# Optimization experiments

Hardware: AMD Instinct MI355X
Metric: run time of the kernel (lower is better)

## Reference

```python
import jax, jax.numpy as jnp
import numpy as np

B, DIM, H, W = 2, 192, 64, 64
HEADS = 4
EPS = 1e-12  # torch F.normalize eps


def conv2d(x, w, groups=1):
    # x: NCHW, w: OIHW, stride 1, SAME padding
    return jax.lax.conv_general_dilated(
        x, w, window_strides=(1, 1), padding='SAME',
        feature_group_count=groups,
        dimension_numbers=('NCHW', 'OIHW', 'NCHW'))


def setup_inputs() -> dict:
    key = jax.random.key(0)
    k1, k2, k3, k4 = jax.random.split(key, 4)
    x = jax.random.normal(k1, (B, DIM, H, W), dtype=jnp.float32)
    qkv_w = jax.random.normal(k2, (3 * DIM, DIM, 1, 1), dtype=jnp.float32) * 0.05
    dw_w = jax.random.normal(k3, (3 * DIM, 1, 3, 3), dtype=jnp.float32) * 0.05
    proj_w = jax.random.normal(k4, (DIM, DIM, 1, 1), dtype=jnp.float32) * 0.05
    temperature = jnp.ones((HEADS, 1, 1), dtype=jnp.float32)
    return {'x': x, 'qkv_w': qkv_w, 'dw_w': dw_w, 'proj_w': proj_w,
            'temperature': temperature}


def reference(x, qkv_w, dw_w, proj_w, temperature):
    b, dim, h, w = x.shape
    heads = temperature.shape[0]
    c = dim // heads  # per-head channels

    qkv = conv2d(conv2d(x, qkv_w), dw_w, groups=3 * dim)  # [b, 3*dim, h, w]
    q, k, v = jnp.split(qkv, 3, axis=1)

    def to_heads(t):
        # b (head c) h w -> b head (h w) c
        return t.reshape(b, heads, c, h * w).transpose(0, 1, 3, 2)

    q, k, v = to_heads(q), to_heads(k), to_heads(v)

    def l2norm(t):
        n = jnp.linalg.norm(t, axis=-1, keepdims=True)
        return t / jnp.maximum(n, EPS)

    q = l2norm(q)
    k = l2norm(k)

    # cosine attention with per-head learnable temperature
    attn = jnp.einsum('bnqc,bnkc->bnqk', q, k) * temperature[None]
    attn = jax.nn.softmax(attn, axis=-1)
    out = jnp.einsum('bnqk,bnkc->bnqc', attn, v)  # [b, head, hw, c]

    # b head (h w) c -> b (head c) h w
    out = out.transpose(0, 1, 3, 2).reshape(b, dim, h, w)
    return conv2d(out, proj_w)
```

## Files before the change

### kernel.cpp

```cpp
#include <hip/hip_runtime.h>
#include <cstdint>
#include <cstddef>

#define HW    4096
#define IMG   64
#define DIMC  192
#define NH    4
#define CH    48
#define CPAD  64
#define KVSPLIT 4
#define NTILE (HW / 64 / KVSPLIT)
#define LOG2E 1.4426950408889634f

typedef __bf16 bf16x8 __attribute__((ext_vector_type(8)));
typedef float  f32x4  __attribute__((ext_vector_type(4)));
typedef float  f32x16 __attribute__((ext_vector_type(16)));
typedef unsigned short u16x8 __attribute__((ext_vector_type(8)));
typedef unsigned int   u32x4 __attribute__((ext_vector_type(4)));

#if __has_builtin(__builtin_amdgcn_exp2f)
#define EXP2(x) __builtin_amdgcn_exp2f(x)
#else
#define EXP2(x) exp2f(x)
#endif

__device__ __forceinline__ unsigned short f2bf(float f) {
  unsigned int u = __builtin_bit_cast(unsigned int, f);
  u = (u + 0x7FFFu + ((u >> 16) & 1u)) >> 16;
  return (unsigned short)u;
}
__device__ __forceinline__ float bf2f(unsigned short u) {
  return __builtin_bit_cast(float, (unsigned int)u << 16);
}
__device__ __forceinline__ f32x4 mfma16(bf16x8 a, bf16x8 b, f32x4 c) {
  return __builtin_amdgcn_mfma_f32_16x16x32_bf16(a, b, c, 0, 0, 0);
}
__device__ __forceinline__ f32x16 mfma32(bf16x8 a, bf16x8 b, f32x16 c) {
  return __builtin_amdgcn_mfma_f32_32x32x16_bf16(a, b, c, 0, 0, 0);
}
__device__ __forceinline__ void gl16(const void* g, void* l) {
  __builtin_amdgcn_global_load_lds(
      (const __attribute__((address_space(1))) unsigned int*)g,
      (__attribute__((address_space(3))) unsigned int*)l, 16, 0, 0);
}
__device__ __forceinline__ unsigned int cvtpk(float lo, float hi) {
  unsigned int d;
  asm("v_cvt_pk_bf16_f32 %0, %1, %2" : "=v"(d) : "v"(lo), "v"(hi));
  return d;
}
__device__ __forceinline__ void swap32(unsigned int& a, unsigned int& b) {
  asm("v_permlane32_swap_b32 %0, %1" : "+v"(a), "+v"(b));
}

__global__ __launch_bounds__(256) void pack2_kernel(
    const float* __restrict__ x, const float* __restrict__ qkv_w,
    const float* __restrict__ proj_w, unsigned short* __restrict__ xb,
    unsigned short* __restrict__ wqkv, unsigned short* __restrict__ wproj) {
  const int bx = blockIdx.x, tid = threadIdx.x;
  if (bx < 64) {
    const int half = bx & 1;
    const int gpx = (bx >> 1) * 256 + tid;
    const int b = gpx >> 12, p = gpx & 4095;
    const int ch0 = half * 96;
    const float* src = x + ((size_t)b * DIMC + ch0) * HW + p;
    #pragma unroll
    for (int kc2 = 0; kc2 < 3; ++kc2) {
      const int kc = half * 3 + kc2;
      u16x8 g[4];
      #pragma unroll
      for (int v = 0; v < 4; ++v)
        #pragma unroll
        for (int j = 0; j < 8; ++j)
          g[v][j] = f2bf(src[(size_t)(kc2 * 32 + v * 8 + j) * HW]);
      unsigned short* dst = xb + (((size_t)b * 6 + kc) * HW + p) * 32;
      #pragma unroll
      for (int v = 0; v < 4; ++v) *(u16x8*)(dst + v * 8) = g[v];
    }
  } else {
    const int row = (bx - 64) * 256 + tid;
    if (row < 576) {
      const float* src = qkv_w + (size_t)row * DIMC;
      #pragma unroll
      for (int kc = 0; kc < 6; ++kc) {
        u16x8 g0, g1, g2, g3;
        #pragma unroll
        for (int j = 0; j < 8; ++j) {
          g0[j] = f2bf(src[kc * 32 + j]);      g1[j] = f2bf(src[kc * 32 + 8 + j]);
          g2[j] = f2bf(src[kc * 32 + 16 + j]); g3[j] = f2bf(src[kc * 32 + 24 + j]);
        }
        unsigned short* dst = wqkv + ((size_t)kc * 576 + row) * 32;
        *(u16x8*)dst = g0; *(u16x8*)(dst + 8) = g1;
        *(u16x8*)(dst + 16) = g2; *(u16x8*)(dst + 24) = g3;
      }
    } else {
      const int oc = row - 576;
      const float* src = proj_w + (size_t)oc * DIMC;
      #pragma unroll
      for (int kc = 0; kc < 6; ++kc) {
        u16x8 g0, g1, g2, g3;
        #pragma unroll
        for (int j = 0; j < 8; ++j) {
          g0[j] = f2bf(src[kc * 32 + j]);      g1[j] = f2bf(src[kc * 32 + 8 + j]);
          g2[j] = f2bf(src[kc * 32 + 16 + j]); g3[j] = f2bf(src[kc * 32 + 24 + j]);
        }
        unsigned short* dst = wproj + ((size_t)kc * DIMC + oc) * 32;
        *(u16x8*)dst = g0; *(u16x8*)(dst + 8) = g1;
        *(u16x8*)(dst + 16) = g2; *(u16x8*)(dst + 24) = g3;
      }
    }
  }
}

__global__ __launch_bounds__(256) void qkv_gemm_kernel(
    const unsigned short* __restrict__ xb, const unsigned short* __restrict__ wb,
    unsigned short* __restrict__ Cout) {
  const int tid = threadIdx.x;
  const int lane = tid & 63, wv = tid >> 6;
  const int l15 = lane & 15, l4 = lane >> 4;
  const int ocbase = blockIdx.x * 192;
  const int px0 = blockIdx.y * 64;
  const int b   = blockIdx.z;

  f32x4 acc[3][4];
  #pragma unroll
  for (int s = 0; s < 3; ++s)
    #pragma unroll
    for (int p = 0; p < 4; ++p) acc[s][p] = f32x4{0.f, 0.f, 0.f, 0.f};

  #pragma unroll
  for (int kc = 0; kc < 6; ++kc) {
    const unsigned short* xrow = xb + (((size_t)b * 6 + kc) * HW + px0 + l15) * 32 + l4 * 8;
    bf16x8 Bf[4];
    #pragma unroll
    for (int p = 0; p < 4; ++p) Bf[p] = *(const bf16x8*)(xrow + p * 512);
    #pragma unroll
    for (int s = 0; s < 3; ++s) {
      const int oc = ocbase + s * 64 + wv * 16 + l15;
      const bf16x8 af = *(const bf16x8*)(wb + ((size_t)kc * 576 + oc) * 32 + l4 * 8);
      #pragma unroll
      for (int p = 0; p < 4; ++p) acc[s][p] = mfma16(af, Bf[p], acc[s][p]);
    }
  }
  #pragma unroll
  for (int s = 0; s < 3; ++s) {
    unsigned short* Cb = Cout + ((size_t)b * 576 + ocbase + s * 64 + wv * 16) * HW + px0;
    #pragma unroll
    for (int p = 0; p < 4; ++p)
      #pragma unroll
      for (int r = 0; r < 4; ++r)
        Cb[(size_t)(l4 * 4 + r) * HW + p * 16 + l15] = f2bf(acc[s][p][r]);
  }
}

__global__ __launch_bounds__(256) void dw_conv3_kernel(
    const unsigned short* __restrict__ X, const float* __restrict__ W,
    unsigned short* __restrict__ Y) {
  __shared__ float T[66][72];
  const int bc = blockIdx.x;
  const int ch = bc % 576;
  const int tid = threadIdx.x;
  const unsigned short* Xb = X + (size_t)bc * HW;
  #pragma unroll
  for (int i = 0; i < 4; ++i) {
    const int idx = i * 256 + tid;
    const int row = idx >> 4, c4 = (idx & 15) << 2;
    const ushort4 u = *(const ushort4*)(Xb + row * 64 + c4);
    float4 f; f.x = bf2f(u.x); f.y = bf2f(u.y); f.z = bf2f(u.z); f.w = bf2f(u.w);
    *(float4*)&T[row + 1][c4 + 4] = f;
  }
  if (tid < 72) { T[0][tid] = 0.f; T[65][tid] = 0.f; }
  if (tid >= 128 && tid < 194) { const int r = tid - 128; T[r][3] = 0.f; T[r][68] = 0.f; }
  float w[9];
  #pragma unroll
  for (int i = 0; i < 9; ++i) w[i] = W[ch * 9 + i];
  __syncthreads();

  const int xx = tid & 63, ys = (tid >> 6) << 4;
  const int c = xx + 4;
  float a0 = T[ys][c - 1],     a1 = T[ys][c],     a2 = T[ys][c + 1];
  float b0 = T[ys + 1][c - 1], b1 = T[ys + 1][c], b2 = T[ys + 1][c + 1];
  unsigned short* Yb = Y + (size_t)bc * HW;
  #pragma unroll
  for (int k = 0; k < 16; ++k) {
    const float c0 = T[ys + k + 2][c - 1], c1 = T[ys + k + 2][c], c2 = T[ys + k + 2][c + 1];
    const float s = w[0] * a0 + w[1] * a1 + w[2] * a2
                  + w[3] * b0 + w[4] * b1 + w[5] * b2
                  + w[6] * c0 + w[7] * c1 + w[8] * c2;
    Yb[(ys + k) * 64 + xx] = f2bf(s);
    a0 = b0; a1 = b1; a2 = b2; b0 = c0; b1 = c1; b2 = c2;
  }
}

__global__ __launch_bounds__(256) void norm_pack3_kernel(
    const unsigned short* __restrict__ Dw, const float* __restrict__ temp,
    unsigned short* __restrict__ Qr, unsigned short* __restrict__ Kr,
    unsigned short* __restrict__ Vs) {
  const int px = blockIdx.x * 256 + threadIdx.x;
  const int sel = blockIdx.y >> 2, h = blockIdx.y & 3;
  const int b = blockIdx.z;
  const int bh = b * NH + h;
  const unsigned short* base = Dw + ((size_t)b * 576 + sel * DIMC + h * CH) * HW + px;

  float v[CH];
  if (sel == 2) {
    const int kt = px & ~63, kl = px & 63;
    #pragma unroll
    for (int c = 0; c < CH; ++c)
      Vs[((size_t)bh * CH + c) * HW + kt + (kl ^ ((c & 7) << 3))] = base[(size_t)c * HW];
    return;
  }
  float ss = 0.f;
  #pragma unroll
  for (int j = 0; j < CH; ++j) { v[j] = bf2f(base[(size_t)j * HW]); ss += v[j] * v[j]; }
  const u16x8 zz = {0, 0, 0, 0, 0, 0, 0, 0};
  if (sel == 0) {
    const float sc = temp[h] * LOG2E / fmaxf(sqrtf(ss), 1e-12f);
    u16x8 gr[8];
    #pragma unroll
    for (int g = 0; g < 6; ++g)
      #pragma unroll
      for (int j = 0; j < 8; ++j) gr[g][j] = f2bf(v[g * 8 + j] * sc);
    gr[6] = zz; gr[7] = zz;
    unsigned short* qrow = Qr + ((size_t)bh * HW + px) * CPAD;
    #pragma unroll
    for (int g = 0; g < 8; ++g) *(u16x8*)(qrow + g * 8) = gr[g];
  } else {
    const int ksw = (px & 3) | (((px >> 3) & 1) << 2);
    const float sc = 1.0f / fmaxf(sqrtf(ss), 1e-12f);
    u16x8 gr[8];
    #pragma unroll
    for (int g = 0; g < 6; ++g)
      #pragma unroll
      for (int j = 0; j < 8; ++j) gr[g][j] = f2bf(v[g * 8 + j] * sc);
    gr[6] = zz; gr[7] = zz;
    unsigned short* krow = Kr + ((size_t)bh * HW + px) * CPAD;
    #pragma unroll
    for (int g = 0; g < 8; ++g) *(u16x8*)(krow + (g ^ ksw) * 8) = gr[g];
  }
}

__global__ __launch_bounds__(256, 2) void flash7_kernel(
    const unsigned short* __restrict__ Qr,
    const unsigned short* __restrict__ Kr,
    const unsigned short* __restrict__ Vs,
    const float* __restrict__ temp,
    unsigned short* __restrict__ Opart, float* __restrict__ Lpart) {
  __shared__ __align__(16) union {
    struct { unsigned short Kl[2][4096]; unsigned short Vl[2][4096]; } s;
    float T[256][53];
  } lds;
  const int tid = threadIdx.x;
  const int lane = tid & 63, wv = tid >> 6;
  const int l31 = lane & 31, lhi = lane >> 5;
  const int bh = blockIdx.x, qt = blockIdx.y, sp = blockIdx.z;
  const int qb = qt * 256 + wv * 64;
  const float m = fabsf(temp[bh & 3]) * LOG2E * 1.05f + 0.1f;

  for (int i = tid; i < 1024; i += 256) {
    const unsigned short vv = (i < 64) ? (unsigned short)0x3F80 : (unsigned short)0;
    lds.s.Vl[0][3072 + i] = vv;
    lds.s.Vl[1][3072 + i] = vv;
  }

  const unsigned short* Qb = Qr + ((size_t)bh * HW + qb) * CPAD;
  bf16x8 qf[2][3];
  #pragma unroll
  for (int qb2 = 0; qb2 < 2; ++qb2)
    #pragma unroll
    for (int ci = 0; ci < 3; ++ci)
      qf[qb2][ci] = *(const bf16x8*)(Qb + (size_t)(qb2 * 32 + l31) * CPAD + ci * 16 + lhi * 8);

  const char* kg = (const char*)Kr + ((size_t)bh * HW + (size_t)sp * (HW / KVSPLIT)) * 128;
  const char* vg = (const char*)Vs + (size_t)bh * CH * HW * 2 + (size_t)sp * (HW / KVSPLIT) * 2;
  const int koA = tid * 16;
  const int vgA = (tid >> 3) * 8192 + (tid & 7) * 16;
  const int vgB = (32 + (tid >> 3)) * 8192 + (tid & 7) * 16;

  auto stage = [&](int buf, const char* kp, const char* vp) {
    char* kl = (char*)&lds.s.Kl[buf][0];
    gl16(kp + koA,        kl + koA);
    gl16(kp + 4096 + koA, kl + 4096 + koA);
    char* vl = (char*)&lds.s.Vl[buf][0];
    gl16(vp + vgA, vl + tid * 16);
    if (tid < 128) gl16(vp + vgB, vl + 4096 + tid * 16);
  };

  f32x16 o[2][2];
  #pragma unroll
  for (int cb = 0; cb < 2; ++cb)
    #pragma unroll
    for (int qb2 = 0; qb2 < 2; ++qb2)
      #pragma unroll
      for (int i = 0; i < 16; ++i) o[cb][qb2][i] = 0.f;
  f32x16 zin;
  #pragma unroll
  for (int i = 0; i < 16; ++i) zin[i] = -m;

  stage(0, kg, vg);
  kg += 8192; vg += 128;
  __syncthreads();
  int cur = 0;
  for (int t = 0; t < NTILE; ++t) {
    if (t + 1 < NTILE) { stage(cur ^ 1, kg, vg); kg += 8192; vg += 128; }
    const unsigned short* KL = &lds.s.Kl[cur][0];
    const unsigned short* VL = &lds.s.Vl[cur][0];

    f32x16 S[2][2];
    __builtin_amdgcn_s_setprio(1);
    #pragma unroll
    for (int kb = 0; kb < 2; ++kb) {
      const int krow = kb * 32 + l31;
      const int ksw = (krow & 3) | (((krow >> 3) & 1) << 2);
      bf16x8 kf[3];
      #pragma unroll
      for (int ci = 0; ci < 3; ++ci)
        kf[ci] = *(const bf16x8*)(KL + krow * 64 + (((ci * 2 + lhi) ^ ksw) * 8));
      #pragma unroll
      for (int qb2 = 0; qb2 < 2; ++qb2) {
        f32x16 acc = zin;
        #pragma unroll
        for (int ci = 0; ci < 3; ++ci) acc = mfma32(kf[ci], qf[qb2][ci], acc);
        S[kb][qb2] = acc;
      }
    }
    __builtin_amdgcn_s_setprio(0);

    #pragma unroll
    for (int kb = 0; kb < 2; ++kb)
      #pragma unroll
      for (int qb2 = 0; qb2 < 2; ++qb2)
        #pragma unroll
        for (int i = 0; i < 16; ++i) S[kb][qb2][i] = EXP2(S[kb][qb2][i]);

    #pragma unroll
    for (int kc = 0; kc < 4; ++kc) {
      const int kb = kc >> 1, rb = (kc & 1) * 8;
      bf16x8 pb[2];
      #pragma unroll
      for (int qb2 = 0; qb2 < 2; ++qb2) {
        unsigned int w0 = cvtpk(S[kb][qb2][rb + 0], S[kb][qb2][rb + 1]);
        unsigned int w1 = cvtpk(S[kb][qb2][rb + 2], S[kb][qb2][rb + 3]);
        unsigned int w2 = cvtpk(S[kb][qb2][rb + 4], S[kb][qb2][rb + 5]);
        unsigned int w3 = cvtpk(S[kb][qb2][rb + 6], S[kb][qb2][rb + 7]);
        swap32(w0, w2);
        swap32(w1, w3);
        u32x4 ww = {w0, w1, w2, w3};
        pb[qb2] = __builtin_bit_cast(bf16x8, ww);
      }
      __builtin_amdgcn_s_setprio(1);
      #pragma unroll
      for (int cb = 0; cb < 2; ++cb) {
        const int crow = cb * 32 + l31;
        const bf16x8 vf = *(const bf16x8*)(VL + crow * 64 + (((kc * 2 + lhi) ^ (crow & 7)) * 8));
        #pragma unroll
        for (int qb2 = 0; qb2 < 2; ++qb2) o[cb][qb2] = mfma32(vf, pb[qb2], o[cb][qb2]);
      }
      __builtin_amdgcn_s_setprio(0);
    }
    __syncthreads();
    cur ^= 1;
  }

  #pragma unroll
  for (int cb = 0; cb < 2; ++cb)
    #pragma unroll
    for (int qb2 = 0; qb2 < 2; ++qb2) {
      const int ql = wv * 64 + qb2 * 32 + l31;
      #pragma unroll
      for (int r = 0; r < 16; ++r) {
        const int c = cb * 32 + (r & 3) + 8 * (r >> 2) + 4 * lhi;
        if (c < 48) lds.T[ql][c] = o[cb][qb2][r];
      }
      if (lhi == 0) lds.T[ql][48] = o[1][qb2][8];
    }
  __syncthreads();
  {
    const int ql = tid;
    const int qg = qt * 256 + ql;
    float vv[48];
    #pragma unroll
    for (int c = 0; c < 48; ++c) vv[c] = lds.T[ql][c];
    const float L = lds.T[ql][48];
    unsigned short* Ob = Opart + ((size_t)(sp * 8 + bh) * HW + qg) * 48;
    #pragma unroll
    for (int g = 0; g < 6; ++g) {
      u16x8 gg;
      #pragma unroll
      for (int j = 0; j < 8; ++j) gg[j] = f2bf(vv[g * 8 + j]);
      *(u16x8*)(Ob + g * 8) = gg;
    }
    Lpart[(size_t)(sp * 8 + bh) * HW + qg] = L;
  }
}

__global__ __launch_bounds__(256) void proj_gemm_kernel(
    const unsigned short* __restrict__ Opart, const float* __restrict__ Lpart,
    const unsigned short* __restrict__ wb, float* __restrict__ Cout) {
  const int tid = threadIdx.x;
  const int lane = tid & 63, wv = tid >> 6;
  const int l15 = lane & 15, l4 = lane >> 4;
  const int px0 = blockIdx.y * 32;
  const int b   = blockIdx.z;

  bf16x8 Bf[6][2];
  #pragma unroll
  for (int kc = 0; kc < 6; ++kc) {
    const int ch0 = kc * 32 + l4 * 8;
    const int head = ch0 / 48, off = ch0 % 48;
    #pragma unroll
    for (int p = 0; p < 2; ++p) {
      const int px = px0 + p * 16 + l15;
      float ls = 0.f;
      #pragma unroll
      for (int sp = 0; sp < 4; ++sp)
        ls += Lpart[(size_t)(sp * 8 + b * 4 + head) * HW + px];
      const float inv = 1.f / ls;
      float a8[8] = {};
      #pragma unroll
      for (int sp = 0; sp < 4; ++sp) {
        const u16x8 u = *(const u16x8*)(Opart +
            ((size_t)(sp * 8 + b * 4 + head) * HW + px) * 48 + off);
        #pragma unroll
        for (int j = 0; j < 8; ++j) a8[j] += bf2f(u[j]);
      }
      u16x8 g;
      #pragma unroll
      for (int j = 0; j < 8; ++j) g[j] = f2bf(a8[j] * inv);
      Bf[kc][p] = __builtin_bit_cast(bf16x8, g);
    }
  }
  #pragma unroll
  for (int s = 0; s < 3; ++s) {
    const int oc = s * 64 + wv * 16 + l15;
    f32x4 acc[2];
    #pragma unroll
    for (int p = 0; p < 2; ++p) acc[p] = f32x4{0.f, 0.f, 0.f, 0.f};
    #pragma unroll
    for (int kc = 0; kc < 6; ++kc) {
      const bf16x8 af = *(const bf16x8*)(wb + ((size_t)kc * DIMC + oc) * 32 + l4 * 8);
      #pragma unroll
      for (int p = 0; p < 2; ++p) acc[p] = mfma16(af, Bf[kc][p], acc[p]);
    }
    float* Cb = Cout + ((size_t)b * DIMC + s * 64 + wv * 16) * HW + px0;
    #pragma unroll
    for (int p = 0; p < 2; ++p)
      #pragma unroll
      for (int r = 0; r < 4; ++r)
        Cb[(size_t)(l4 * 4 + r) * HW + p * 16 + l15] = acc[p][r];
  }
}

extern "C" void kernel_launch(void* const* d_in, const int* in_sizes, int n_in,
                              void* d_out, int out_size, void* d_ws, size_t ws_size,
                              hipStream_t stream) {
  const float* x      = (const float*)d_in[0];
  const float* qkv_w  = (const float*)d_in[1];
  const float* dw_w   = (const float*)d_in[2];
  const float* proj_w = (const float*)d_in[3];
  const float* temp   = (const float*)d_in[4];

  char* ws = (char*)d_ws;
  unsigned short* xb    = (unsigned short*)(ws);
  unsigned short* wqkv  = (unsigned short*)(ws + 3145728);
  unsigned short* wproj = (unsigned short*)(ws + 3366912);
  unsigned short* qkvb  = (unsigned short*)(ws + 3440640);
  unsigned short* dwb   = (unsigned short*)(ws + 12877824);
  unsigned short* Qr    = (unsigned short*)(ws + 22315008);
  unsigned short* Kr    = (unsigned short*)(ws + 26509312);
  unsigned short* Vs    = (unsigned short*)(ws + 30703616);
  unsigned short* Opart = (unsigned short*)(ws + 33849344);
  float*          Lpart = (float*)(ws + 46432256);

  pack2_kernel<<<dim3(67), 256, 0, stream>>>(x, qkv_w, proj_w, xb, wqkv, wproj);
  qkv_gemm_kernel<<<dim3(3, 64, 2), 256, 0, stream>>>(xb, wqkv, qkvb);
  dw_conv3_kernel<<<dim3(1152), 256, 0, stream>>>(qkvb, dw_w, dwb);
  norm_pack3_kernel<<<dim3(16, 12, 2), 256, 0, stream>>>(dwb, temp, Qr, Kr, Vs);
  flash7_kernel<<<dim3(8, 16, KVSPLIT), 256, 0, stream>>>(Qr, Kr, Vs, temp, Opart, Lpart);
  proj_gemm_kernel<<<dim3(1, 128, 2), 256, 0, stream>>>(Opart, Lpart, wproj, (float*)d_out);
}
```

Measured before the change: 80.48 us.

## Fuse depthwise conv with L2 normalization and widen input packing grid

Merges the depthwise 3x3 conv kernel and the normalize/pack kernel into one kernel that loads a 4-row halo tile of 48 channels into LDS, convolves it, transposes through LDS, then normalizes and writes Q/K/V. This drops the intermediate dw buffer's global write and read and one launch. The input pack kernel is also reorganized to use 128 blocks with 48-channel groups for more parallelism. The fused kernel launches only 384 blocks, each redoing halo rows and holding large register arrays, which may cut occupancy.

```diff
diff --git a/kernel.cpp b/kernel.cpp
--- a/kernel.cpp
+++ b/kernel.cpp
@@ -52,32 +52,32 @@
   asm("v_permlane32_swap_b32 %0, %1" : "+v"(a), "+v"(b));
 }
 
-__global__ __launch_bounds__(256) void pack2_kernel(
+__global__ __launch_bounds__(256) void pack3_kernel(
     const float* __restrict__ x, const float* __restrict__ qkv_w,
     const float* __restrict__ proj_w, unsigned short* __restrict__ xb,
     unsigned short* __restrict__ wqkv, unsigned short* __restrict__ wproj) {
   const int bx = blockIdx.x, tid = threadIdx.x;
-  if (bx < 64) {
-    const int half = bx & 1;
-    const int gpx = (bx >> 1) * 256 + tid;
-    const int b = gpx >> 12, p = gpx & 4095;
-    const int ch0 = half * 96;
-    const float* src = x + ((size_t)b * DIMC + ch0) * HW + p;
-    #pragma unroll
-    for (int kc2 = 0; kc2 < 3; ++kc2) {
-      const int kc = half * 3 + kc2;
-      u16x8 g[4];
-      #pragma unroll
-      for (int v = 0; v < 4; ++v)
-        #pragma unroll
-        for (int j = 0; j < 8; ++j)
-          g[v][j] = f2bf(src[(size_t)(kc2 * 32 + v * 8 + j) * HW]);
-      unsigned short* dst = xb + (((size_t)b * 6 + kc) * HW + p) * 32;
-      #pragma unroll
-      for (int v = 0; v < 4; ++v) *(u16x8*)(dst + v * 8) = g[v];
+  if (bx < 128) {
+    const int it = bx * 256 + tid;
+    const int b = it >> 14;
+    const int q4 = (it >> 12) & 3;
+    const int p = it & 4095;
+    const int c0 = q4 * 48;
+    const float* src = x + ((size_t)b * DIMC + c0) * HW + p;
+    float v[48];
+    #pragma unroll
+    for (int j = 0; j < 48; ++j) v[j] = src[(size_t)j * HW];
+    #pragma unroll
+    for (int g = 0; g < 6; ++g) {
+      const int ch = c0 + g * 8;
+      const int kc = ch >> 5, off = ch & 31;
+      u16x8 gg;
+      #pragma unroll
+      for (int j = 0; j < 8; ++j) gg[j] = f2bf(v[g * 8 + j]);
+      *(u16x8*)(xb + (((size_t)b * 6 + kc) * HW + p) * 32 + off) = gg;
     }
   } else {
-    const int row = (bx - 64) * 256 + tid;
+    const int row = (bx - 128) * 256 + tid;
     if (row < 576) {
       const float* src = qkv_w + (size_t)row * DIMC;
       #pragma unroll
@@ -152,66 +152,87 @@
   }
 }
 
-__global__ __launch_bounds__(256) void dw_conv3_kernel(
-    const unsigned short* __restrict__ X, const float* __restrict__ W,
-    unsigned short* __restrict__ Y) {
-  __shared__ float T[66][72];
-  const int bc = blockIdx.x;
-  const int ch = bc % 576;
-  const int tid = threadIdx.x;
-  const unsigned short* Xb = X + (size_t)bc * HW;
-  #pragma unroll
-  for (int i = 0; i < 4; ++i) {
-    const int idx = i * 256 + tid;
-    const int row = idx >> 4, c4 = (idx & 15) << 2;
-    const ushort4 u = *(const ushort4*)(Xb + row * 64 + c4);
-    float4 f; f.x = bf2f(u.x); f.y = bf2f(u.y); f.z = bf2f(u.z); f.w = bf2f(u.w);
-    *(float4*)&T[row + 1][c4 + 4] = f;
-  }
-  if (tid < 72) { T[0][tid] = 0.f; T[65][tid] = 0.f; }
-  if (tid >= 128 && tid < 194) { const int r = tid - 128; T[r][3] = 0.f; T[r][68] = 0.f; }
-  float w[9];
-  #pragma unroll
-  for (int i = 0; i < 9; ++i) w[i] = W[ch * 9 + i];
-  __syncthreads();
-
-  const int xx = tid & 63, ys = (tid >> 6) << 4;
-  const int c = xx + 4;
-  float a0 = T[ys][c - 1],     a1 = T[ys][c],     a2 = T[ys][c + 1];
-  float b0 = T[ys + 1][c - 1], b1 = T[ys + 1][c], b2 = T[ys + 1][c + 1];
-  unsigned short* Yb = Y + (size_t)bc * HW;
-  #pragma unroll
-  for (int k = 0; k < 16; ++k) {
-    const float c0 = T[ys + k + 2][c - 1], c1 = T[ys + k + 2][c], c2 = T[ys + k + 2][c + 1];
-    const float s = w[0] * a0 + w[1] * a1 + w[2] * a2
-                  + w[3] * b0 + w[4] * b1 + w[5] * b2
-                  + w[6] * c0 + w[7] * c1 + w[8] * c2;
-    Yb[(ys + k) * 64 + xx] = f2bf(s);
-    a0 = b0; a1 = b1; a2 = b2; b0 = c0; b1 = c1; b2 = c2;
-  }
-}
-
-__global__ __launch_bounds__(256) void norm_pack3_kernel(
-    const unsigned short* __restrict__ Dw, const float* __restrict__ temp,
+__global__ __launch_bounds__(256) void dwnorm_kernel(
+    const unsigned short* __restrict__ qkvb, const float* __restrict__ dw_w,
+    const float* __restrict__ temp,
     unsigned short* __restrict__ Qr, unsigned short* __restrict__ Kr,
     unsigned short* __restrict__ Vs) {
-  const int px = blockIdx.x * 256 + threadIdx.x;
+  __shared__ union {
+    unsigned short IN[48][6][64];
+    float OUT[4][64][49];
+  } L;
+  const int tid = threadIdx.x;
+  const int y0 = blockIdx.x * 4;
   const int sel = blockIdx.y >> 2, h = blockIdx.y & 3;
-  const int b = blockIdx.z;
-  const int bh = b * NH + h;
-  const unsigned short* base = Dw + ((size_t)b * 576 + sel * DIMC + h * CH) * HW + px;
+  const int b = blockIdx.z, bh = b * NH + h;
+  const int cbase = sel * DIMC + h * CH;
+
+  #pragma unroll
+  for (int i = 0; i < 9; ++i) {
+    const int idx = i * 256 + tid;
+    const int ch = idx / 48;
+    const int rem = idx % 48;
+    const int r = rem >> 3, pxg = rem & 7;
+    const int y = y0 - 1 + r;
+    u16x8 v = {0, 0, 0, 0, 0, 0, 0, 0};
+    if (y >= 0 && y < IMG)
+      v = *(const u16x8*)(qkvb + ((size_t)(b * 576 + cbase + ch)) * HW + y * 64 + pxg * 8);
+    *(u16x8*)(&L.IN[ch][r][pxg * 8]) = v;
+  }
+  __syncthreads();
+
+  const int px = tid & 63, cg = tid >> 6;
+  const int chg = cg * 12;
+  float out[12][4];
+  #pragma unroll
+  for (int cc = 0; cc < 12; ++cc) {
+    const int gch = cbase + chg + cc;
+    float w[9];
+    #pragma unroll
+    for (int i = 0; i < 9; ++i) w[i] = dw_w[gch * 9 + i];
+    float a0 = (px > 0)  ? bf2f(L.IN[chg + cc][0][px - 1]) : 0.f;
+    float a1 =             bf2f(L.IN[chg + cc][0][px]);
+    float a2 = (px < 63) ? bf2f(L.IN[chg + cc][0][px + 1]) : 0.f;
+    float b0 = (px > 0)  ? bf2f(L.IN[chg + cc][1][px - 1]) : 0.f;
+    float b1 =             bf2f(L.IN[chg + cc][1][px]);
+    float b2 = (px < 63) ? bf2f(L.IN[chg + cc][1][px + 1]) : 0.f;
+    #pragma unroll
+    for (int k = 0; k < 4; ++k) {
+      const float c0 = (px > 0)  ? bf2f(L.IN[chg + cc][k + 2][px - 1]) : 0.f;
+      const float c1 =             bf2f(L.IN[chg + cc][k + 2][px]);
+      const float c2 = (px < 63) ? bf2f(L.IN[chg + cc][k + 2][px + 1]) : 0.f;
+      out[cc][k] = w[0] * a0 + w[1] * a1 + w[2] * a2
+                 + w[3] * b0 + w[4] * b1 + w[5] * b2
+                 + w[6] * c0 + w[7] * c1 + w[8] * c2;
+      a0 = b0; a1 = b1; a2 = b2; b0 = c0; b1 = c1; b2 = c2;
+    }
+  }
+
+  if (sel == 2) {
+    #pragma unroll
+    for (int cc = 0; cc < 12; ++cc) {
+      const int c = chg + cc;
+      #pragma unroll
+      for (int k = 0; k < 4; ++k)
+        Vs[((size_t)bh * CH + c) * HW + (y0 + k) * 64 + (px ^ ((c & 7) << 3))] =
+            f2bf(out[cc][k]);
+    }
+    return;
+  }
+
+  __syncthreads();
+  #pragma unroll
+  for (int cc = 0; cc < 12; ++cc)
+    #pragma unroll
+    for (int k = 0; k < 4; ++k)
+      L.OUT[k][px][chg + cc] = out[cc][k];
+  __syncthreads();
 
   float v[CH];
-  if (sel == 2) {
-    const int kt = px & ~63, kl = px & 63;
-    #pragma unroll
-    for (int c = 0; c < CH; ++c)
-      Vs[((size_t)bh * CH + c) * HW + kt + (kl ^ ((c & 7) << 3))] = base[(size_t)c * HW];
-    return;
-  }
   float ss = 0.f;
   #pragma unroll
-  for (int j = 0; j < CH; ++j) { v[j] = bf2f(base[(size_t)j * HW]); ss += v[j] * v[j]; }
+  for (int c = 0; c < CH; ++c) { v[c] = L.OUT[cg][px][c]; ss += v[c] * v[c]; }
+  const int p = (y0 + cg) * 64 + px;
   const u16x8 zz = {0, 0, 0, 0, 0, 0, 0, 0};
   if (sel == 0) {
     const float sc = temp[h] * LOG2E / fmaxf(sqrtf(ss), 1e-12f);
@@ -221,11 +242,11 @@
       #pragma unroll
       for (int j = 0; j < 8; ++j) gr[g][j] = f2bf(v[g * 8 + j] * sc);
     gr[6] = zz; gr[7] = zz;
-    unsigned short* qrow = Qr + ((size_t)bh * HW + px) * CPAD;
+    unsigned short* qrow = Qr + ((size_t)bh * HW + p) * CPAD;
     #pragma unroll
     for (int g = 0; g < 8; ++g) *(u16x8*)(qrow + g * 8) = gr[g];
   } else {
-    const int ksw = (px & 3) | (((px >> 3) & 1) << 2);
+    const int ksw = (p & 3) | (((p >> 3) & 1) << 2);
     const float sc = 1.0f / fmaxf(sqrtf(ss), 1e-12f);
     u16x8 gr[8];
     #pragma unroll
@@ -233,7 +254,7 @@
       #pragma unroll
       for (int j = 0; j < 8; ++j) gr[g][j] = f2bf(v[g * 8 + j] * sc);
     gr[6] = zz; gr[7] = zz;
-    unsigned short* krow = Kr + ((size_t)bh * HW + px) * CPAD;
+    unsigned short* krow = Kr + ((size_t)bh * HW + p) * CPAD;
     #pragma unroll
     for (int g = 0; g < 8; ++g) *(u16x8*)(krow + (g ^ ksw) * 8) = gr[g];
   }
@@ -380,7 +401,7 @@
     float vv[48];
     #pragma unroll
     for (int c = 0; c < 48; ++c) vv[c] = lds.T[ql][c];
-    const float L = lds.T[ql][48];
+    const float Lv = lds.T[ql][48];
     unsigned short* Ob = Opart + ((size_t)(sp * 8 + bh) * HW + qg) * 48;
     #pragma unroll
     for (int g = 0; g < 6; ++g) {
@@ -389,7 +410,7 @@
       for (int j = 0; j < 8; ++j) gg[j] = f2bf(vv[g * 8 + j]);
       *(u16x8*)(Ob + g * 8) = gg;
     }
-    Lpart[(size_t)(sp * 8 + bh) * HW + qg] = L;
+    Lpart[(size_t)(sp * 8 + bh) * HW + qg] = Lv;
   }
 }
 
@@ -464,17 +485,15 @@
   unsigned short* wqkv  = (unsigned short*)(ws + 3145728);
   unsigned short* wproj = (unsigned short*)(ws + 3366912);
   unsigned short* qkvb  = (unsigned short*)(ws + 3440640);
-  unsigned short* dwb   = (unsigned short*)(ws + 12877824);
-  unsigned short* Qr    = (unsigned short*)(ws + 22315008);
-  unsigned short* Kr    = (unsigned short*)(ws + 26509312);
-  unsigned short* Vs    = (unsigned short*)(ws + 30703616);
-  unsigned short* Opart = (unsigned short*)(ws + 33849344);
-  float*          Lpart = (float*)(ws + 46432256);
-
-  pack2_kernel<<<dim3(67), 256, 0, stream>>>(x, qkv_w, proj_w, xb, wqkv, wproj);
+  unsigned short* Qr    = (unsigned short*)(ws + 12877824);
+  unsigned short* Kr    = (unsigned short*)(ws + 17072128);
+  unsigned short* Vs    = (unsigned short*)(ws + 21266432);
+  unsigned short* Opart = (unsigned short*)(ws + 24412160);
+  float*          Lpart = (float*)(ws + 36995072);
+
+  pack3_kernel<<<dim3(131), 256, 0, stream>>>(x, qkv_w, proj_w, xb, wqkv, wproj);
   qkv_gemm_kernel<<<dim3(3, 64, 2), 256, 0, stream>>>(xb, wqkv, qkvb);
-  dw_conv3_kernel<<<dim3(1152), 256, 0, stream>>>(qkvb, dw_w, dwb);
-  norm_pack3_kernel<<<dim3(16, 12, 2), 256, 0, stream>>>(dwb, temp, Qr, Kr, Vs);
+  dwnorm_kernel<<<dim3(16, 12, 2), 256, 0, stream>>>(qkvb, dw_w, temp, Qr, Kr, Vs);
   flash7_kernel<<<dim3(8, 16, KVSPLIT), 256, 0, stream>>>(Qr, Kr, Vs, temp, Opart, Lpart);
   proj_gemm_kernel<<<dim3(1, 128, 2), 256, 0, stream>>>(Opart, Lpart, wproj, (float*)d_out);
 }
```

Measured after the change: 92.00 us. +14.3%, slower.
